# Performance work log

Measured on AMD Instinct MI355X. Metric: run time of the kernel, lower is better.

Reference implementation:

```python
import jax, jax.numpy as jnp
import numpy as np

B, C, H, W = 8, 64, 112, 112
KEY_NUM = 9


def conv1x1(x, w, b):
    # x: [b,c,h,w], w: [co,ci], b: [co]
    return jnp.einsum('bchw,oc->bohw', x, w) + b[None, :, None, None]


def bilinear_sample(feat, dy, dx):
    # feat: [b,c,H,W]; dy,dx: [b,H,W]. Zero-padded bilinear point sampling
    # (equivalent to torchvision deform_conv2d with 1x1 identity weight).
    b, c, h, w = feat.shape
    yy = jnp.arange(h, dtype=feat.dtype)[:, None]
    xx = jnp.arange(w, dtype=feat.dtype)[None, :]
    py = dy + yy  # [b,h,w]
    px = dx + xx
    y0 = jnp.floor(py)
    x0 = jnp.floor(px)
    wy1 = py - y0
    wx1 = px - x0
    wy0 = 1.0 - wy1
    wx0 = 1.0 - wx1
    featf = feat.reshape(b, c, h * w)

    def gather(yi, xi):
        valid = (yi >= 0) & (yi < h) & (xi >= 0) & (xi < w)
        yc = jnp.clip(yi, 0, h - 1).astype(jnp.int32)
        xc = jnp.clip(xi, 0, w - 1).astype(jnp.int32)
        idx = (yc * w + xc).reshape(b, 1, h * w)
        v = jnp.take_along_axis(featf, idx, axis=2).reshape(b, c, h, w)
        return v * valid.astype(feat.dtype)[:, None]

    return (gather(y0, x0) * (wy0 * wx0)[:, None]
            + gather(y0, x0 + 1) * (wy0 * wx1)[:, None]
            + gather(y0 + 1, x0) * (wy1 * wx0)[:, None]
            + gather(y0 + 1, x0 + 1) * (wy1 * wx1)[:, None])


def setup_inputs() -> dict:
    key = jax.random.key(0)
    ks = jax.random.split(key, 8)
    s = 1.0 / np.sqrt(C)
    return {
        'query_layer': jax.random.normal(ks[0], (B, C, H, W), jnp.float32),
        'key_layer': jax.random.normal(ks[1], (B, C, H, W), jnp.float32),
        'w_refer': jax.random.normal(ks[2], (C, C), jnp.float32) * s,
        'b_refer': jax.random.normal(ks[3], (C,), jnp.float32) * 0.1,
        'w_attn': jax.random.normal(ks[4], (KEY_NUM, C), jnp.float32) * s,
        'b_attn': jax.random.normal(ks[5], (KEY_NUM,), jnp.float32) * 0.1,
        'w_off': jax.random.normal(ks[6], (2 * KEY_NUM, C), jnp.float32) * s,
        'b_off': jax.random.normal(ks[7], (2 * KEY_NUM,), jnp.float32) * 0.1,
    }


def reference(query_layer, key_layer, w_refer, b_refer, w_attn, b_attn, w_off, b_off):
    key_feature = conv1x1(key_layer, w_refer, b_refer)          # [b,c,h,w]
    attn = jax.nn.softmax(conv1x1(query_layer, w_attn, b_attn), axis=1)  # [b,K,h,w]
    offset = conv1x1(query_layer, w_off, b_off)                  # [b,2K,h,w]
    # Faithful to original: key k uses offset channels [k, k+1] (overlapping slices)
    dys = jnp.moveaxis(offset[:, 0:KEY_NUM], 1, 0)               # [K,b,h,w]
    dxs = jnp.moveaxis(offset[:, 1:KEY_NUM + 1], 1, 0)           # [K,b,h,w]
    sampled = jax.vmap(bilinear_sample, in_axes=(None, 0, 0))(key_feature, dys, dxs)  # [K,b,c,h,w]
    out = jnp.einsum('kbchw,bkhw->bchw', sampled, attn)
    return out
```

## Files before the change

### kernel.cpp

```cpp
#include <hip/hip_runtime.h>
#include <hip/hip_fp16.h>

#define BB 8
#define CC 64
#define HH 112
#define WW 112
#define HWs (HH * WW)
#define KEYN 9

#define CK_PX 128
#define CK_TILES (HWs / CK_PX)
#define CK_NBLK (BB * CK_TILES)
#define WTS 68

#define SM_PX 32
#define SM_TILES (HWs / SM_PX)
#define SM_NBLK (BB * SM_TILES)

#define OFF_WQ   0
#define OFF_SB   1280
#define OFF_L    1300
#define OFF_XQ   1972
#define OFF_P    0
#define OFF_T    0
#define OFF_OUTT 2304
#define SM_LDS   4480

typedef int v4i __attribute__((ext_vector_type(4)));

#define GLOAD(dst, p) asm volatile("global_load_dwordx4 %0, %1, off" \
                                   : "=&v"(dst) : "v"(p))

__device__ __forceinline__ float swzx16(float v) {
    return __uint_as_float(__builtin_amdgcn_ds_swizzle(__float_as_uint(v), 0x401F));
}
__device__ __forceinline__ float swzx8(float v) {
    return __uint_as_float(__builtin_amdgcn_ds_swizzle(__float_as_uint(v), 0x201F));
}

__global__ __launch_bounds__(256, 3) void conv_key_kernel(
    const float* __restrict__ key, const float* __restrict__ w_refer,
    const float* __restrict__ b_refer, __half* __restrict__ Kf)
{
    __shared__ float Xin[64 * CK_PX];
    __shared__ float Wt[64 * WTS];

    const int t = threadIdx.x;
    const int blk = blockIdx.x;
    const int b = blk & 7;
    const int s0 = (blk >> 3) * CK_PX;
    const size_t inb = (size_t)b * CC * HWs + s0;

    #pragma unroll
    for (int m = 0; m < 4; ++m) {
        const int f = t + 256 * m;
        const int o = f >> 4;
        const int q = f & 15;
        const float4 wv = *reinterpret_cast<const float4*>(w_refer + o * CC + 4 * q);
        Wt[(4 * q + 0) * WTS + o] = wv.x;
        Wt[(4 * q + 1) * WTS + o] = wv.y;
        Wt[(4 * q + 2) * WTS + o] = wv.z;
        Wt[(4 * q + 3) * WTS + o] = wv.w;
    }
    #pragma unroll
    for (int m = 0; m < 8; ++m) {
        const int f = t + 256 * m;
        const int k = f >> 5;
        const int p8 = f & 31;
        *reinterpret_cast<float4*>(&Xin[k * CK_PX + 4 * p8]) =
            *reinterpret_cast<const float4*>(key + inb + (size_t)k * HWs + 4 * p8);
    }
    __syncthreads();

    const int og = t & 7;
    const int p4 = t >> 3;
    const float4 bias0 = *reinterpret_cast<const float4*>(b_refer + 8 * og);
    const float4 bias1 = *reinterpret_cast<const float4*>(b_refer + 8 * og + 4);
    float4 acc[4][2];
    #pragma unroll
    for (int pi = 0; pi < 4; ++pi) { acc[pi][0] = bias0; acc[pi][1] = bias1; }

    #pragma unroll 4
    for (int k = 0; k < 64; ++k) {
        const float4 a4 = *reinterpret_cast<const float4*>(&Xin[k * CK_PX + 4 * p4]);
        const float4 w0 = *reinterpret_cast<const float4*>(&Wt[k * WTS + 8 * og]);
        const float4 w1 = *reinterpret_cast<const float4*>(&Wt[k * WTS + 8 * og + 4]);
        const float ap[4] = {a4.x, a4.y, a4.z, a4.w};
        #pragma unroll
        for (int pi = 0; pi < 4; ++pi) {
            acc[pi][0].x = fmaf(ap[pi], w0.x, acc[pi][0].x);
            acc[pi][0].y = fmaf(ap[pi], w0.y, acc[pi][0].y);
            acc[pi][0].z = fmaf(ap[pi], w0.z, acc[pi][0].z);
            acc[pi][0].w = fmaf(ap[pi], w0.w, acc[pi][0].w);
            acc[pi][1].x = fmaf(ap[pi], w1.x, acc[pi][1].x);
            acc[pi][1].y = fmaf(ap[pi], w1.y, acc[pi][1].y);
            acc[pi][1].z = fmaf(ap[pi], w1.z, acc[pi][1].z);
            acc[pi][1].w = fmaf(ap[pi], w1.w, acc[pi][1].w);
        }
    }

    #pragma unroll
    for (int pi = 0; pi < 4; ++pi) {
        const size_t ob = ((size_t)b * HWs + s0 + 4 * p4 + pi) * CC + 8 * og;
        union { __half2 h; int i; } u0, u1, u2, u3;
        u0.h = __floats2half2_rn(acc[pi][0].x, acc[pi][0].y);
        u1.h = __floats2half2_rn(acc[pi][0].z, acc[pi][0].w);
        u2.h = __floats2half2_rn(acc[pi][1].x, acc[pi][1].y);
        u3.h = __floats2half2_rn(acc[pi][1].z, acc[pi][1].w);
        int4 pk; pk.x = u0.i; pk.y = u1.i; pk.z = u2.i; pk.w = u3.i;
        *reinterpret_cast<int4*>(Kf + ob) = pk;
    }
}

struct TEnt { float4 a, b; };

__device__ __forceinline__ TEnt make_entry2(int e, float4 pk, int s0)
{
    const int p = e & 31;
    const int s = s0 + p;
    const int yi = s / WW;
    const int xi = s - yi * WW;
    const float py  = pk.y + (float)yi;
    const float pxf = pk.z + (float)xi;
    const float fy = floorf(py), fx = floorf(pxf);
    const float wy1 = py - fy, wx1 = pxf - fx;
    const float wy0 = 1.f - wy1, wx0 = 1.f - wx1;
    const int ix0 = (int)fx;
    const int iy0 = (int)fy, iy1 = iy0 + 1;
    const float vx0 = (ix0 >= 0 && ix0 < WW)      ? 1.f : 0.f;
    const float vx1 = (ix0 >= -1 && ix0 < WW - 1) ? 1.f : 0.f;
    const float vy0 = (iy0 >= 0 && iy0 < HH)      ? 1.f : 0.f;
    const float vy1 = (iy1 >= 0 && iy1 < HH)      ? 1.f : 0.f;
    const int yc0 = min(max(iy0, 0), HH - 1);
    const int yc1 = min(max(iy1, 0), HH - 1);
    TEnt r;
    r.a.x = __uint_as_float((unsigned)(yc0 * WW * 128));
    r.a.y = __uint_as_float((unsigned)(yc1 * WW * 128));
    r.a.z = __int_as_float(ix0);
    r.a.w = 0.f;
    const float ay0 = pk.x * wy0 * vy0;
    const float ay1 = pk.x * wy1 * vy1;
    r.b.x = ay0 * wx0 * vx0;
    r.b.y = ay0 * wx1 * vx1;
    r.b.z = ay1 * wx0 * vx0;
    r.b.w = ay1 * wx1 * vx1;
    return r;
}

__global__ __launch_bounds__(256, 4) void fused_sample_kernel(
    const float* __restrict__ query, const float* __restrict__ w_attn,
    const float* __restrict__ b_attn, const float* __restrict__ w_off,
    const float* __restrict__ b_off, const __half* __restrict__ Kf,
    float* __restrict__ out)
{
    __shared__ float S[SM_LDS];
    float*  Wq   = S + OFF_WQ;
    float*  Sb   = S + OFF_SB;
    float*  L    = S + OFF_L;
    float*  Xq   = S + OFF_XQ;
    float4* Pf4  = reinterpret_cast<float4*>(S + OFF_P);
    float*  Tb   = S + OFF_T;
    float*  OutT = S + OFF_OUTT;

    const int t = threadIdx.x;
    const int l = t & 63;
    const int w = t >> 6;
    const int blk = blockIdx.x;
    const int b = blk & 7;
    const int tile = blk >> 3;
    const int s0 = tile * SM_PX;
    const size_t qb = (size_t)b * CC * HWs + s0;
    const char* Kfb = reinterpret_cast<const char*>(Kf) + (size_t)b * HWs * 128;

    for (int f = t; f < 304; f += 256) {
        const int r = f >> 4;
        const int q = f & 15;
        const float* src = (r < KEYN) ? (w_attn + r * CC) : (w_off + (r - KEYN) * CC);
        const float4 wv = *reinterpret_cast<const float4*>(src + 4 * q);
        Wq[(4 * q + 0) * 20 + r] = wv.x;
        Wq[(4 * q + 1) * 20 + r] = wv.y;
        Wq[(4 * q + 2) * 20 + r] = wv.z;
        Wq[(4 * q + 3) * 20 + r] = wv.w;
    }
    if (t < 64) Wq[t * 20 + 19] = 0.f;
    if (t < 20) Sb[t] = (t < KEYN) ? b_attn[t] : (t < 19 ? b_off[t - KEYN] : 0.f);
    #pragma unroll
    for (int m = 0; m < 2; ++m) {
        const int f = t + 256 * m;
        const int c = f >> 3;
        const int p4 = (f & 7) * 4;
        *reinterpret_cast<float4*>(&Xq[c * 32 + p4]) =
            *reinterpret_cast<const float4*>(query + qb + (size_t)c * HWs + p4);
    }
    __syncthreads();

    {
        const int px = t & 31;
        const int og = t >> 5;
        if (og < 5) {
            const int o4 = 4 * og;
            float4 acc = *reinterpret_cast<const float4*>(&Sb[o4]);
            #pragma unroll 8
            for (int k = 0; k < 64; ++k) {
                const float a = Xq[k * 32 + px];
                const float4 wv = *reinterpret_cast<const float4*>(&Wq[k * 20 + o4]);
                acc.x = fmaf(a, wv.x, acc.x);
                acc.y = fmaf(a, wv.y, acc.y);
                acc.z = fmaf(a, wv.z, acc.z);
                acc.w = fmaf(a, wv.w, acc.w);
            }
            L[px * 21 + o4 + 0] = acc.x;
            L[px * 21 + o4 + 1] = acc.y;
            L[px * 21 + o4 + 2] = acc.z;
            L[px * 21 + o4 + 3] = acc.w;
        }
    }
    __syncthreads();

    if (t < SM_PX) {
        float lg[KEYN], of[10];
        #pragma unroll
        for (int k = 0; k < KEYN; ++k) lg[k] = L[t * 21 + k];
        #pragma unroll
        for (int j = 0; j < 10; ++j) of[j] = L[t * 21 + KEYN + j];
        float m = lg[0];
        #pragma unroll
        for (int k = 1; k < KEYN; ++k) m = fmaxf(m, lg[k]);
        float s = 0.f, e[KEYN];
        #pragma unroll
        for (int k = 0; k < KEYN; ++k) { e[k] = expf(lg[k] - m); s += e[k]; }
        const float sinv = 1.0f / s;
        #pragma unroll
        for (int k = 0; k < KEYN; ++k)
            Pf4[k * 32 + t] = make_float4(e[k] * sinv, of[k], of[k + 1], 0.f);
    }
    __syncthreads();

    {
        const float4 q1 = Pf4[t];
        float4 q2 = make_float4(0.f, 0.f, 0.f, 0.f);
        if (t < 32) q2 = Pf4[256 + t];
        __syncthreads();
        #pragma unroll
        for (int m = 0; m < 2; ++m) {
            const int e = (m == 0) ? t : (256 + t);
            if (m == 1 && t >= 32) break;
            const TEnt en = make_entry2(e, (m == 0) ? q1 : q2, s0);
            const int p = e & 31, k = e >> 5;
            const int x0 = __float_as_int(en.a.z);
            const unsigned xc0 = (unsigned)(min(max(x0, 0), WW - 1)) << 7;
            const unsigned xc1 = (unsigned)(min(max(x0 + 1, 0), WW - 1)) << 7;
            const unsigned rb0 = __float_as_uint(en.a.x);
            const unsigned rb1 = __float_as_uint(en.a.y);
            float4 r0, r1;
            r0.x = __uint_as_float(rb0 + xc0); r0.y = en.b.x;
            r0.z = __uint_as_float(rb0 + xc1); r0.w = en.b.y;
            r1.x = __uint_as_float(rb1 + xc0); r1.y = en.b.z;
            r1.z = __uint_as_float(rb1 + xc1); r1.w = en.b.w;
            float* dst = Tb + (p * 9 + k) * 8;
            *reinterpret_cast<float4*>(dst)     = r0;
            *reinterpret_cast<float4*>(dst + 4) = r1;
        }
    }
    __syncthreads();

    const int  ch8  = l & 7;
    const int  corf = ((l >> 3) & 3) * 2;
    const int  sub  = l >> 5;
    const char* KfbC = Kfb + (unsigned)(ch8 * 16);

    for (int j = 0; j < 4; ++j) {
        const int p = w * 8 + 2 * j + sub;
        const float* Te = Tb + p * 72 + corf;

        float2 tw[KEYN];
        #pragma unroll
        for (int k = 0; k < KEYN; ++k)
            tw[k] = *reinterpret_cast<const float2*>(Te + k * 8);

        v4i rr[KEYN];
        #pragma unroll
        for (int k = 0; k < KEYN; ++k)
            GLOAD(rr[k], KfbC + __float_as_uint(tw[k].x));
        asm volatile("s_waitcnt vmcnt(0)" ::: "memory");
        __builtin_amdgcn_sched_barrier(0);

        float acc[8] = {0.f, 0.f, 0.f, 0.f, 0.f, 0.f, 0.f, 0.f};
        #pragma unroll
        for (int k = 0; k < KEYN; ++k) {
            const float wgt = tw[k].y;
            union { int i; __half2 h; } u0, u1, u2, u3;
            u0.i = rr[k][0]; u1.i = rr[k][1]; u2.i = rr[k][2]; u3.i = rr[k][3];
            acc[0] = fmaf(__low2float(u0.h),  wgt, acc[0]);
            acc[1] = fmaf(__high2float(u0.h), wgt, acc[1]);
            acc[2] = fmaf(__low2float(u1.h),  wgt, acc[2]);
            acc[3] = fmaf(__high2float(u1.h), wgt, acc[3]);
            acc[4] = fmaf(__low2float(u2.h),  wgt, acc[4]);
            acc[5] = fmaf(__high2float(u2.h), wgt, acc[5]);
            acc[6] = fmaf(__low2float(u3.h),  wgt, acc[6]);
            acc[7] = fmaf(__high2float(u3.h), wgt, acc[7]);
        }

        #pragma unroll
        for (int i = 0; i < 8; ++i) acc[i] += swzx16(acc[i]);
        #pragma unroll
        for (int i = 0; i < 8; ++i) acc[i] += swzx8(acc[i]);

        if ((l & 24) == 0) {
            float* d = OutT + p * 68 + ch8 * 8;
            *reinterpret_cast<float4*>(d)     = make_float4(acc[0], acc[1], acc[2], acc[3]);
            *reinterpret_cast<float4*>(d + 4) = make_float4(acc[4], acc[5], acc[6], acc[7]);
        }
    }
    __syncthreads();

    const size_t ob = (size_t)b * CC * HWs + s0;
    #pragma unroll
    for (int m = 0; m < 8; ++m) {
        const int f = t + 256 * m;
        const int c = f >> 5;
        const int px = f & 31;
        out[ob + (size_t)c * HWs + px] = OutT[px * 68 + c];
    }
}

extern "C" void kernel_launch(void* const* d_in, const int* in_sizes, int n_in,
                              void* d_out, int out_size, void* d_ws, size_t ws_size,
                              hipStream_t stream)
{
    const float* query   = (const float*)d_in[0];
    const float* key     = (const float*)d_in[1];
    const float* w_refer = (const float*)d_in[2];
    const float* b_refer = (const float*)d_in[3];
    const float* w_attn  = (const float*)d_in[4];
    const float* b_attn  = (const float*)d_in[5];
    const float* w_off   = (const float*)d_in[6];
    const float* b_off   = (const float*)d_in[7];
    float* out = (float*)d_out;

    __half* Kf = (__half*)d_ws;

    hipLaunchKernelGGL(conv_key_kernel, dim3(CK_NBLK), dim3(256), 0, stream,
                       key, w_refer, b_refer, Kf);
    hipLaunchKernelGGL(fused_sample_kernel, dim3(SM_NBLK), dim3(256), 0, stream,
                       query, w_attn, b_attn, w_off, b_off, Kf, out);
}
```

Measured before the change: 147.1 us.

## Double-buffer gather loads in sampler and reorder conv block-to-batch mapping

The four-iteration gather loop in the sampling kernel becomes a two-stage software pipeline. The next pixel's nine gathers are issued before the current pixel's are consumed, waiting with vmcnt(9) rather than draining all loads, so memory latency overlaps the FMA and reduction work. This costs more VGPRs, which may pressure the occupancy target of 4. Separately, the key-conv kernel now maps consecutive blocks to consecutive spatial tiles within one batch instead of interleaving batches.

```diff
diff --git a/kernel.cpp b/kernel.cpp
--- a/kernel.cpp
+++ b/kernel.cpp
@@ -47,8 +47,8 @@
 
     const int t = threadIdx.x;
     const int blk = blockIdx.x;
-    const int b = blk & 7;
-    const int s0 = (blk >> 3) * CK_PX;
+    const int b = blk / CK_TILES;
+    const int s0 = (blk - b * CK_TILES) * CK_PX;
     const size_t inb = (size_t)b * CC * HWs + s0;
 
     #pragma unroll
@@ -147,6 +147,54 @@
     return r;
 }
 
+#define READ_TW(twv, p) do {                                                  \
+    const float* Te_ = Tb + (p) * 72 + corf;                                  \
+    _Pragma("unroll")                                                         \
+    for (int k = 0; k < KEYN; ++k)                                            \
+        twv[k] = *reinterpret_cast<const float2*>(Te_ + k * 8);               \
+} while (0)
+
+#define ISSUE9(rrv, twv) do {                                                 \
+    _Pragma("unroll")                                                         \
+    for (int k = 0; k < KEYN; ++k)                                            \
+        GLOAD(rrv[k], KfbC + __float_as_uint(twv[k].x));                      \
+} while (0)
+
+#define CONSUME(twv, rrv, p) do {                                             \
+    float acc_[8] = {0.f, 0.f, 0.f, 0.f, 0.f, 0.f, 0.f, 0.f};                 \
+    _Pragma("unroll")                                                         \
+    for (int k = 0; k < KEYN; ++k) {                                          \
+        const float wgt_ = twv[k].y;                                          \
+        union { int i; __half2 h; } u0_, u1_, u2_, u3_;                       \
+        u0_.i = rrv[k][0]; u1_.i = rrv[k][1];                                 \
+        u2_.i = rrv[k][2]; u3_.i = rrv[k][3];                                 \
+        acc_[0] = fmaf(__low2float(u0_.h),  wgt_, acc_[0]);                   \
+        acc_[1] = fmaf(__high2float(u0_.h), wgt_, acc_[1]);                   \
+        acc_[2] = fmaf(__low2float(u1_.h),  wgt_, acc_[2]);                   \
+        acc_[3] = fmaf(__high2float(u1_.h), wgt_, acc_[3]);                   \
+        acc_[4] = fmaf(__low2float(u2_.h),  wgt_, acc_[4]);                   \
+        acc_[5] = fmaf(__high2float(u2_.h), wgt_, acc_[5]);                   \
+        acc_[6] = fmaf(__low2float(u3_.h),  wgt_, acc_[6]);                   \
+        acc_[7] = fmaf(__high2float(u3_.h), wgt_, acc_[7]);                   \
+    }                                                                         \
+    _Pragma("unroll")                                                         \
+    for (int i = 0; i < 8; ++i) acc_[i] += swzx16(acc_[i]);                   \
+    _Pragma("unroll")                                                         \
+    for (int i = 0; i < 8; ++i) acc_[i] += swzx8(acc_[i]);                    \
+    if ((l & 24) == 0) {                                                      \
+        float* d_ = OutT + (p) * 68 + ch8 * 8;                                \
+        *reinterpret_cast<float4*>(d_)     =                                  \
+            make_float4(acc_[0], acc_[1], acc_[2], acc_[3]);                  \
+        *reinterpret_cast<float4*>(d_ + 4) =                                  \
+            make_float4(acc_[4], acc_[5], acc_[6], acc_[7]);                  \
+    }                                                                         \
+} while (0)
+
+#define WAITN(n) do {                                                         \
+    asm volatile("s_waitcnt vmcnt(" #n ")" ::: "memory");                     \
+    __builtin_amdgcn_sched_barrier(0);                                        \
+} while (0)
+
 __global__ __launch_bounds__(256, 4) void fused_sample_kernel(
     const float* __restrict__ query, const float* __restrict__ w_attn,
     const float* __restrict__ b_attn, const float* __restrict__ w_off,
@@ -268,49 +316,24 @@
     const int  corf = ((l >> 3) & 3) * 2;
     const int  sub  = l >> 5;
     const char* KfbC = Kfb + (unsigned)(ch8 * 16);
-
-    for (int j = 0; j < 4; ++j) {
-        const int p = w * 8 + 2 * j + sub;
-        const float* Te = Tb + p * 72 + corf;
-
-        float2 tw[KEYN];
-        #pragma unroll
-        for (int k = 0; k < KEYN; ++k)
-            tw[k] = *reinterpret_cast<const float2*>(Te + k * 8);
-
-        v4i rr[KEYN];
-        #pragma unroll
-        for (int k = 0; k < KEYN; ++k)
-            GLOAD(rr[k], KfbC + __float_as_uint(tw[k].x));
-        asm volatile("s_waitcnt vmcnt(0)" ::: "memory");
-        __builtin_amdgcn_sched_barrier(0);
-
-        float acc[8] = {0.f, 0.f, 0.f, 0.f, 0.f, 0.f, 0.f, 0.f};
-        #pragma unroll
-        for (int k = 0; k < KEYN; ++k) {
-            const float wgt = tw[k].y;
-            union { int i; __half2 h; } u0, u1, u2, u3;
-            u0.i = rr[k][0]; u1.i = rr[k][1]; u2.i = rr[k][2]; u3.i = rr[k][3];
-            acc[0] = fmaf(__low2float(u0.h),  wgt, acc[0]);
-            acc[1] = fmaf(__high2float(u0.h), wgt, acc[1]);
-            acc[2] = fmaf(__low2float(u1.h),  wgt, acc[2]);
-            acc[3] = fmaf(__high2float(u1.h), wgt, acc[3]);
-            acc[4] = fmaf(__low2float(u2.h),  wgt, acc[4]);
-            acc[5] = fmaf(__high2float(u2.h), wgt, acc[5]);
-            acc[6] = fmaf(__low2float(u3.h),  wgt, acc[6]);
-            acc[7] = fmaf(__high2float(u3.h), wgt, acc[7]);
-        }
-
-        #pragma unroll
-        for (int i = 0; i < 8; ++i) acc[i] += swzx16(acc[i]);
-        #pragma unroll
-        for (int i = 0; i < 8; ++i) acc[i] += swzx8(acc[i]);
-
-        if ((l & 24) == 0) {
-            float* d = OutT + p * 68 + ch8 * 8;
-            *reinterpret_cast<float4*>(d)     = make_float4(acc[0], acc[1], acc[2], acc[3]);
-            *reinterpret_cast<float4*>(d + 4) = make_float4(acc[4], acc[5], acc[6], acc[7]);
-        }
+    const int  pw   = w * 8 + sub;
+
+    {
+        float2 twA[KEYN], twB[KEYN];
+        v4i    rrA[KEYN], rrB[KEYN];
+
+        READ_TW(twA, pw + 0); ISSUE9(rrA, twA);
+        READ_TW(twB, pw + 2); ISSUE9(rrB, twB);
+        WAITN(9);
+        CONSUME(twA, rrA, pw + 0);
+        READ_TW(twA, pw + 4); ISSUE9(rrA, twA);
+        WAITN(9);
+        CONSUME(twB, rrB, pw + 2);
+        READ_TW(twB, pw + 6); ISSUE9(rrB, twB);
+        WAITN(9);
+        CONSUME(twA, rrA, pw + 4);
+        WAITN(0);
+        CONSUME(twB, rrB, pw + 6);
     }
     __syncthreads();
 
```

Result: no change. 145.3 us (-1.2%).

## Retile key 1x1 conv to 256-pixel blocks with register-prefetched K chunks

Applied to the files above, without the earlier changes.

The key-projection conv now handles 256 pixels per block, and each thread computes an 8x8 register tile where it used to compute 4x8. Input channels are staged through shared memory in chunks of 16, and the next chunk is prefetched into registers from global memory while the current one is computed. This cuts the shared-memory footprint and aims for more FMAs per LDS load and better latency hiding, with occupancy raised to 4 blocks per unit. The costs are higher register pressure from 64 accumulators plus the prefetch buffer, extra barriers, and half as many blocks in the grid.

```diff
diff --git a/kernel.cpp b/kernel.cpp
--- a/kernel.cpp
+++ b/kernel.cpp
@@ -8,9 +8,9 @@
 #define HWs (HH * WW)
 #define KEYN 9
 
-#define CK_PX 128
-#define CK_TILES (HWs / CK_PX)
-#define CK_NBLK (BB * CK_TILES)
+#define CK2_PX 256
+#define CK2_TILES (HWs / CK2_PX)
+#define CK2_NBLK (BB * CK2_TILES)
 #define WTS 68
 
 #define SM_PX 32
@@ -38,17 +38,17 @@
     return __uint_as_float(__builtin_amdgcn_ds_swizzle(__float_as_uint(v), 0x201F));
 }
 
-__global__ __launch_bounds__(256, 3) void conv_key_kernel(
+__global__ __launch_bounds__(256, 4) void conv_key_kernel(
     const float* __restrict__ key, const float* __restrict__ w_refer,
     const float* __restrict__ b_refer, __half* __restrict__ Kf)
 {
-    __shared__ float Xin[64 * CK_PX];
     __shared__ float Wt[64 * WTS];
+    __shared__ float Xin[16 * CK2_PX];
 
     const int t = threadIdx.x;
     const int blk = blockIdx.x;
-    const int b = blk & 7;
-    const int s0 = (blk >> 3) * CK_PX;
+    const int b = blk / CK2_TILES;
+    const int s0 = (blk - b * CK2_TILES) * CK2_PX;
     const size_t inb = (size_t)b * CC * HWs + s0;
 
     #pragma unroll
@@ -63,50 +63,79 @@
         Wt[(4 * q + 3) * WTS + o] = wv.w;
     }
     #pragma unroll
-    for (int m = 0; m < 8; ++m) {
+    for (int m = 0; m < 4; ++m) {
         const int f = t + 256 * m;
-        const int k = f >> 5;
-        const int p8 = f & 31;
-        *reinterpret_cast<float4*>(&Xin[k * CK_PX + 4 * p8]) =
-            *reinterpret_cast<const float4*>(key + inb + (size_t)k * HWs + 4 * p8);
+        const int kr = f >> 6;
+        const int c4 = (f & 63) * 4;
+        *reinterpret_cast<float4*>(&Xin[kr * CK2_PX + c4]) =
+            *reinterpret_cast<const float4*>(key + inb + (size_t)kr * HWs + c4);
     }
     __syncthreads();
 
     const int og = t & 7;
-    const int p4 = t >> 3;
-    const float4 bias0 = *reinterpret_cast<const float4*>(b_refer + 8 * og);
-    const float4 bias1 = *reinterpret_cast<const float4*>(b_refer + 8 * og + 4);
-    float4 acc[4][2];
-    #pragma unroll
-    for (int pi = 0; pi < 4; ++pi) { acc[pi][0] = bias0; acc[pi][1] = bias1; }
-
-    #pragma unroll 4
-    for (int k = 0; k < 64; ++k) {
-        const float4 a4 = *reinterpret_cast<const float4*>(&Xin[k * CK_PX + 4 * p4]);
-        const float4 w0 = *reinterpret_cast<const float4*>(&Wt[k * WTS + 8 * og]);
-        const float4 w1 = *reinterpret_cast<const float4*>(&Wt[k * WTS + 8 * og + 4]);
-        const float ap[4] = {a4.x, a4.y, a4.z, a4.w};
-        #pragma unroll
-        for (int pi = 0; pi < 4; ++pi) {
-            acc[pi][0].x = fmaf(ap[pi], w0.x, acc[pi][0].x);
-            acc[pi][0].y = fmaf(ap[pi], w0.y, acc[pi][0].y);
-            acc[pi][0].z = fmaf(ap[pi], w0.z, acc[pi][0].z);
-            acc[pi][0].w = fmaf(ap[pi], w0.w, acc[pi][0].w);
-            acc[pi][1].x = fmaf(ap[pi], w1.x, acc[pi][1].x);
-            acc[pi][1].y = fmaf(ap[pi], w1.y, acc[pi][1].y);
-            acc[pi][1].z = fmaf(ap[pi], w1.z, acc[pi][1].z);
-            acc[pi][1].w = fmaf(ap[pi], w1.w, acc[pi][1].w);
-        }
-    }
-
-    #pragma unroll
-    for (int pi = 0; pi < 4; ++pi) {
-        const size_t ob = ((size_t)b * HWs + s0 + 4 * p4 + pi) * CC + 8 * og;
+    const int pg = t >> 3;
+
+    float acc[8][8];
+    {
+        const float4 b0 = *reinterpret_cast<const float4*>(b_refer + 8 * og);
+        const float4 b1 = *reinterpret_cast<const float4*>(b_refer + 8 * og + 4);
+        #pragma unroll
+        for (int pi = 0; pi < 8; ++pi) {
+            acc[pi][0] = b0.x; acc[pi][1] = b0.y; acc[pi][2] = b0.z; acc[pi][3] = b0.w;
+            acc[pi][4] = b1.x; acc[pi][5] = b1.y; acc[pi][6] = b1.z; acc[pi][7] = b1.w;
+        }
+    }
+
+    float4 pf[4];
+    #pragma unroll
+    for (int kc = 0; kc < 4; ++kc) {
+        if (kc < 3) {
+            #pragma unroll
+            for (int m = 0; m < 4; ++m) {
+                const int f = t + 256 * m;
+                const int kr = f >> 6;
+                const int c4 = (f & 63) * 4;
+                pf[m] = *reinterpret_cast<const float4*>(
+                    key + inb + (size_t)((kc + 1) * 16 + kr) * HWs + c4);
+            }
+        }
+        #pragma unroll 4
+        for (int kk = 0; kk < 16; ++kk) {
+            const float4 a0 = *reinterpret_cast<const float4*>(&Xin[kk * CK2_PX + pg * 8]);
+            const float4 a1 = *reinterpret_cast<const float4*>(&Xin[kk * CK2_PX + pg * 8 + 4]);
+            const int k = kc * 16 + kk;
+            const float4 w0 = *reinterpret_cast<const float4*>(&Wt[k * WTS + og * 8]);
+            const float4 w1 = *reinterpret_cast<const float4*>(&Wt[k * WTS + og * 8 + 4]);
+            const float av[8] = {a0.x, a0.y, a0.z, a0.w, a1.x, a1.y, a1.z, a1.w};
+            const float wv[8] = {w0.x, w0.y, w0.z, w0.w, w1.x, w1.y, w1.z, w1.w};
+            #pragma unroll
+            for (int pi = 0; pi < 8; ++pi) {
+                #pragma unroll
+                for (int oj = 0; oj < 8; ++oj)
+                    acc[pi][oj] = fmaf(av[pi], wv[oj], acc[pi][oj]);
+            }
+        }
+        __syncthreads();
+        if (kc < 3) {
+            #pragma unroll
+            for (int m = 0; m < 4; ++m) {
+                const int f = t + 256 * m;
+                const int kr = f >> 6;
+                const int c4 = (f & 63) * 4;
+                *reinterpret_cast<float4*>(&Xin[kr * CK2_PX + c4]) = pf[m];
+            }
+            __syncthreads();
+        }
+    }
+
+    #pragma unroll
+    for (int pi = 0; pi < 8; ++pi) {
+        const size_t ob = ((size_t)b * HWs + s0 + pg * 8 + pi) * CC + 8 * og;
         union { __half2 h; int i; } u0, u1, u2, u3;
-        u0.h = __floats2half2_rn(acc[pi][0].x, acc[pi][0].y);
-        u1.h = __floats2half2_rn(acc[pi][0].z, acc[pi][0].w);
-        u2.h = __floats2half2_rn(acc[pi][1].x, acc[pi][1].y);
-        u3.h = __floats2half2_rn(acc[pi][1].z, acc[pi][1].w);
+        u0.h = __floats2half2_rn(acc[pi][0], acc[pi][1]);
+        u1.h = __floats2half2_rn(acc[pi][2], acc[pi][3]);
+        u2.h = __floats2half2_rn(acc[pi][4], acc[pi][5]);
+        u3.h = __floats2half2_rn(acc[pi][6], acc[pi][7]);
         int4 pk; pk.x = u0.i; pk.y = u1.i; pk.z = u2.i; pk.w = u3.i;
         *reinterpret_cast<int4*>(Kf + ob) = pk;
     }
@@ -340,7 +369,7 @@
 
     __half* Kf = (__half*)d_ws;
 
-    hipLaunchKernelGGL(conv_key_kernel, dim3(CK_NBLK), dim3(256), 0, stream,
+    hipLaunchKernelGGL(conv_key_kernel, dim3(CK2_NBLK), dim3(256), 0, stream,
                        key, w_refer, b_refer, Kf);
     hipLaunchKernelGGL(fused_sample_kernel, dim3(SM_NBLK), dim3(256), 0, stream,
                        query, w_attn, b_attn, w_off, b_off, Kf, out);
```

Result: no change. 147.7 us (+0.4%).

## Compute key 1x1 conv with fp16 MFMA instead of fp32 FMA loop

Applied to the files above, without the earlier changes.

Rewrites the key projection kernel to use 16x16x32 fp16 MFMA instructions. Weights are converted to half in LDS, and key activations are loaded straight from global memory into half registers without LDS staging. The aim is to cut the VALU FMA cost and LDS traffic of the conv stage, and occupancy is raised via launch bounds. In exchange the conv inputs lose precision (fp16 weights and activations), and the strided per-element global loads may coalesce less well.

```diff
diff --git a/kernel.cpp b/kernel.cpp
--- a/kernel.cpp
+++ b/kernel.cpp
@@ -8,10 +8,10 @@
 #define HWs (HH * WW)
 #define KEYN 9
 
-#define CK_PX 128
-#define CK_TILES (HWs / CK_PX)
-#define CK_NBLK (BB * CK_TILES)
-#define WTS 68
+#define CKM_PX 128
+#define CKM_TILES (HWs / CKM_PX)
+#define CKM_NBLK (BB * CKM_TILES)
+#define WTH 72
 
 #define SM_PX 32
 #define SM_TILES (HWs / SM_PX)
@@ -26,7 +26,9 @@
 #define OFF_OUTT 2304
 #define SM_LDS   4480
 
-typedef int v4i __attribute__((ext_vector_type(4)));
+typedef int   v4i __attribute__((ext_vector_type(4)));
+typedef float v4f __attribute__((ext_vector_type(4)));
+typedef _Float16 v8h __attribute__((ext_vector_type(8)));
 
 #define GLOAD(dst, p) asm volatile("global_load_dwordx4 %0, %1, off" \
                                    : "=&v"(dst) : "v"(p))
@@ -38,17 +40,16 @@
     return __uint_as_float(__builtin_amdgcn_ds_swizzle(__float_as_uint(v), 0x201F));
 }
 
-__global__ __launch_bounds__(256, 3) void conv_key_kernel(
+__global__ __launch_bounds__(256, 4) void conv_key_kernel(
     const float* __restrict__ key, const float* __restrict__ w_refer,
     const float* __restrict__ b_refer, __half* __restrict__ Kf)
 {
-    __shared__ float Xin[64 * CK_PX];
-    __shared__ float Wt[64 * WTS];
+    __shared__ __half Wt[64 * WTH];
 
     const int t = threadIdx.x;
     const int blk = blockIdx.x;
     const int b = blk & 7;
-    const int s0 = (blk >> 3) * CK_PX;
+    const int s0 = (blk >> 3) * CKM_PX;
     const size_t inb = (size_t)b * CC * HWs + s0;
 
     #pragma unroll
@@ -57,58 +58,57 @@
         const int o = f >> 4;
         const int q = f & 15;
         const float4 wv = *reinterpret_cast<const float4*>(w_refer + o * CC + 4 * q);
-        Wt[(4 * q + 0) * WTS + o] = wv.x;
-        Wt[(4 * q + 1) * WTS + o] = wv.y;
-        Wt[(4 * q + 2) * WTS + o] = wv.z;
-        Wt[(4 * q + 3) * WTS + o] = wv.w;
-    }
-    #pragma unroll
-    for (int m = 0; m < 8; ++m) {
-        const int f = t + 256 * m;
-        const int k = f >> 5;
-        const int p8 = f & 31;
-        *reinterpret_cast<float4*>(&Xin[k * CK_PX + 4 * p8]) =
-            *reinterpret_cast<const float4*>(key + inb + (size_t)k * HWs + 4 * p8);
-    }
-    __syncthreads();
-
-    const int og = t & 7;
-    const int p4 = t >> 3;
-    const float4 bias0 = *reinterpret_cast<const float4*>(b_refer + 8 * og);
-    const float4 bias1 = *reinterpret_cast<const float4*>(b_refer + 8 * og + 4);
-    float4 acc[4][2];
-    #pragma unroll
-    for (int pi = 0; pi < 4; ++pi) { acc[pi][0] = bias0; acc[pi][1] = bias1; }
-
-    #pragma unroll 4
-    for (int k = 0; k < 64; ++k) {
-        const float4 a4 = *reinterpret_cast<const float4*>(&Xin[k * CK_PX + 4 * p4]);
-        const float4 w0 = *reinterpret_cast<const float4*>(&Wt[k * WTS + 8 * og]);
-        const float4 w1 = *reinterpret_cast<const float4*>(&Wt[k * WTS + 8 * og + 4]);
-        const float ap[4] = {a4.x, a4.y, a4.z, a4.w};
-        #pragma unroll
-        for (int pi = 0; pi < 4; ++pi) {
-            acc[pi][0].x = fmaf(ap[pi], w0.x, acc[pi][0].x);
-            acc[pi][0].y = fmaf(ap[pi], w0.y, acc[pi][0].y);
-            acc[pi][0].z = fmaf(ap[pi], w0.z, acc[pi][0].z);
-            acc[pi][0].w = fmaf(ap[pi], w0.w, acc[pi][0].w);
-            acc[pi][1].x = fmaf(ap[pi], w1.x, acc[pi][1].x);
-            acc[pi][1].y = fmaf(ap[pi], w1.y, acc[pi][1].y);
-            acc[pi][1].z = fmaf(ap[pi], w1.z, acc[pi][1].z);
-            acc[pi][1].w = fmaf(ap[pi], w1.w, acc[pi][1].w);
-        }
-    }
-
-    #pragma unroll
-    for (int pi = 0; pi < 4; ++pi) {
-        const size_t ob = ((size_t)b * HWs + s0 + 4 * p4 + pi) * CC + 8 * og;
-        union { __half2 h; int i; } u0, u1, u2, u3;
-        u0.h = __floats2half2_rn(acc[pi][0].x, acc[pi][0].y);
-        u1.h = __floats2half2_rn(acc[pi][0].z, acc[pi][0].w);
-        u2.h = __floats2half2_rn(acc[pi][1].x, acc[pi][1].y);
-        u3.h = __floats2half2_rn(acc[pi][1].z, acc[pi][1].w);
-        int4 pk; pk.x = u0.i; pk.y = u1.i; pk.z = u2.i; pk.w = u3.i;
-        *reinterpret_cast<int4*>(Kf + ob) = pk;
+        __half2* dst = reinterpret_cast<__half2*>(&Wt[o * WTH + 4 * q]);
+        dst[0] = __floats2half2_rn(wv.x, wv.y);
+        dst[1] = __floats2half2_rn(wv.z, wv.w);
+    }
+    __syncthreads();
+
+    const int l  = t & 63;
+    const int w  = t >> 6;
+    const int lo = l & 15;
+    const int hi = l >> 4;
+    const int px0 = w * 32;
+
+    v8h aW[4][2];
+    #pragma unroll
+    for (int ot = 0; ot < 4; ++ot)
+        #pragma unroll
+        for (int ks = 0; ks < 2; ++ks)
+            aW[ot][ks] = *reinterpret_cast<const v8h*>(
+                &Wt[(ot * 16 + lo) * WTH + ks * 32 + hi * 8]);
+
+    v8h bK[2][2];
+    #pragma unroll
+    for (int pt = 0; pt < 2; ++pt) {
+        const int px = px0 + pt * 16 + lo;
+        #pragma unroll
+        for (int ks = 0; ks < 2; ++ks) {
+            const float* kp = key + inb + (size_t)(ks * 32 + hi * 8) * HWs + px;
+            v8h bb;
+            #pragma unroll
+            for (int j = 0; j < 8; ++j)
+                bb[j] = (_Float16)kp[(size_t)j * HWs];
+            bK[pt][ks] = bb;
+        }
+    }
+
+    #pragma unroll
+    for (int ot = 0; ot < 4; ++ot) {
+        const float4 bv = *reinterpret_cast<const float4*>(b_refer + ot * 16 + hi * 4);
+        #pragma unroll
+        for (int pt = 0; pt < 2; ++pt) {
+            v4f c;
+            c[0] = bv.x; c[1] = bv.y; c[2] = bv.z; c[3] = bv.w;
+            c = __builtin_amdgcn_mfma_f32_16x16x32_f16(aW[ot][0], bK[pt][0], c, 0, 0, 0);
+            c = __builtin_amdgcn_mfma_f32_16x16x32_f16(aW[ot][1], bK[pt][1], c, 0, 0, 0);
+            const int px = px0 + pt * 16 + lo;
+            const size_t ob = ((size_t)b * HWs + s0 + px) * CC + ot * 16 + hi * 4;
+            union { __half2 h[2]; float2 f; } u;
+            u.h[0] = __floats2half2_rn(c[0], c[1]);
+            u.h[1] = __floats2half2_rn(c[2], c[3]);
+            *reinterpret_cast<float2*>(Kf + ob) = u.f;
+        }
     }
 }
 
@@ -340,7 +340,7 @@
 
     __half* Kf = (__half*)d_ws;
 
-    hipLaunchKernelGGL(conv_key_kernel, dim3(CK_NBLK), dim3(256), 0, stream,
+    hipLaunchKernelGGL(conv_key_kernel, dim3(CKM_NBLK), dim3(256), 0, stream,
                        key, w_refer, b_refer, Kf);
     hipLaunchKernelGGL(fused_sample_kernel, dim3(SM_NBLK), dim3(256), 0, stream,
                        query, w_attn, b_attn, w_off, b_off, Kf, out);
```

Measured after the change: 137.8 us (median of 2 runs). 6.4% less time.
